# Kernel tuning notes

Measured on AMD Instinct MI355X. Metric: run time of the kernel, lower is better.

Reference implementation:

```python
import math
import jax, jax.numpy as jnp
import numpy as np


def _expmap0(u):
    # geoopt Lorentz (k=1) expmap0 followed by projection back onto the hyperboloid.
    # Minkowski norm of the tangent input (geoopt clamps at 1e-8 before sqrt).
    u0 = u[..., :1]
    us = u[..., 1:]
    mink = -u0 * u0 + jnp.sum(us * us, axis=-1, keepdims=True)
    nomin = jnp.sqrt(jnp.maximum(mink, 1e-8))
    r = jnp.sinh(nomin) * u / nomin
    space = r[..., 1:]
    time = jnp.sqrt(1.0 + jnp.sum(space * space, axis=-1, keepdims=True))  # project()
    return jnp.concatenate([time, space], axis=-1)


def setup_inputs() -> dict:
    key = jax.random.key(0)
    B, T, E, H = 2, 1024, 1024, 16
    ks = jax.random.split(key, 8)
    s = 0.02
    return {
        "x": jax.random.normal(ks[0], (B, T, E), jnp.float32),
        "Wqkv": jax.random.normal(ks[1], (3 * E, E), jnp.float32) * s,
        "bqkv": jnp.zeros((3 * E,), jnp.float32),
        "Wout": jax.random.normal(ks[2], (E, E), jnp.float32) * s,
        "bout": jnp.zeros((E,), jnp.float32),
        "Wimp": jax.random.normal(ks[3], (1, E), jnp.float32) * s,
        "bimp": jnp.zeros((1,), jnp.float32),
        "Walpha": jax.random.normal(ks[4], (H, E), jnp.float32) * s,
        "balpha": jnp.zeros((H,), jnp.float32),
        "spike_threshold": jnp.asarray(0.5, jnp.float32),
        "log_k": jnp.full((H,), 0.54, jnp.float32),
        "qk_scale": jnp.asarray(0.1, jnp.float32),
    }


def reference(x, Wqkv, bqkv, Wout, bout, Wimp, bimp, Walpha, balpha,
              spike_threshold, log_k, qk_scale):
    B, T, C = x.shape
    H = log_k.shape[0]
    D = C // H

    importance = jax.nn.sigmoid(x @ Wimp.T + bimp)          # (B,T,1)
    # torch.tril on the (T,1) trailing dims keeps every element -> no-op mask.
    spikes = (importance > spike_threshold).astype(x.dtype)
    spike_mask = spikes.reshape(B, 1, T, 1)

    alpha = jax.nn.sigmoid(x @ Walpha.T + balpha)           # (B,T,H)
    alpha = jnp.transpose(alpha, (0, 2, 1))[..., None]      # (B,H,T,1)

    qkv = (x @ Wqkv.T + bqkv).reshape(B, T, 3, H, D)
    q = jnp.transpose(qkv[:, :, 0], (0, 2, 1, 3))           # (B,H,T,D)
    k = jnp.transpose(qkv[:, :, 1], (0, 2, 1, 3))
    v = jnp.transpose(qkv[:, :, 2], (0, 2, 1, 3))

    scores_euclid = jnp.einsum('bhtd,bhsd->bhts', q, k) / math.sqrt(D)

    safe_scale = jax.nn.sigmoid(qk_scale) * 1.5
    qn = q / jnp.maximum(jnp.linalg.norm(q, axis=-1, keepdims=True), 1e-12) * safe_scale
    kn = k / jnp.maximum(jnp.linalg.norm(k, axis=-1, keepdims=True), 1e-12) * safe_scale
    q_hyp = _expmap0(qn)
    k_hyp = _expmap0(kn)

    inner = (-jnp.einsum('bhti,bhsi->bhts', q_hyp[..., :1], k_hyp[..., :1])
             + jnp.einsum('bhtd,bhsd->bhts', q_hyp[..., 1:], k_hyp[..., 1:]))
    curv_k = (jax.nn.softplus(log_k) + 1e-6).reshape(1, H, 1, 1)
    mdot = jnp.maximum(-inner, 1.0 + 1e-6)
    dist = jnp.arccosh(mdot)
    scores_hyper = -(dist * dist) / curv_k

    scores = (1.0 - alpha) * scores_euclid + alpha * scores_hyper
    causal = jnp.tril(jnp.ones((T, T), bool))
    scores = jnp.where(causal[None, None], scores, -jnp.inf)

    attn = jax.nn.softmax(scores, axis=-1) * spike_mask     # dropout disabled (eval)
    y = jnp.einsum('bhts,bhsd->bhtd', attn, v)
    y = jnp.transpose(y, (0, 2, 1, 3)).reshape(B, T, C)
    return y @ Wout.T + bout
```

## Files before the change

kernel.cpp:

```cpp
#include <hip/hip_runtime.h>
#include <math.h>

#define B_ 2
#define T_ 1024
#define E_ 1024
#define H_ 16
#define D_ 64
#define M_ (B_*T_)
#define SPLANE 32768

typedef __bf16 bf16x8 __attribute__((ext_vector_type(8)));
typedef __bf16 bf16x4 __attribute__((ext_vector_type(4)));
typedef __bf16 bf16x2 __attribute__((ext_vector_type(2)));
typedef float f32x4 __attribute__((ext_vector_type(4)));

__device__ __forceinline__ void* ldsp(__bf16* base, int row, int byte) {
  return (char*)base + row * 128 + (byte ^ ((row & 7) << 4));
}

__device__ __forceinline__ void gload_lds16(const void* g, void* l) {
  __builtin_amdgcn_global_load_lds((const __attribute__((address_space(1))) void*)g,
                                   (__attribute__((address_space(3))) void*)l, 16, 0, 0);
}

#define XV4 524288
#define WQV4 786432
#define WOV4 262144
#define TOTV4 (XV4 + WQV4 + WOV4)
__global__ __launch_bounds__(256) void conv_kernel(
    const float* __restrict__ x, const float* __restrict__ Wqkv,
    const float* __restrict__ Wout,
    __bf16* __restrict__ xb, __bf16* __restrict__ Wqkvb, __bf16* __restrict__ Woutb) {
  for (size_t i = (size_t)blockIdx.x * blockDim.x + threadIdx.x; i < TOTV4;
       i += (size_t)gridDim.x * blockDim.x) {
    const float4* src; __bf16* dst; size_t off;
    if (i < XV4)            { src = (const float4*)x;    dst = xb;    off = i; }
    else if (i < XV4+WQV4)  { src = (const float4*)Wqkv; dst = Wqkvb; off = i - XV4; }
    else                    { src = (const float4*)Wout; dst = Woutb; off = i - XV4 - WQV4; }
    float4 val = src[off];
    bf16x4 o = {(__bf16)val.x, (__bf16)val.y, (__bf16)val.z, (__bf16)val.w};
    *(bf16x4*)(dst + off * 4) = o;
  }
}

__global__ __launch_bounds__(256) void imp_alpha_kernel(
    const float* __restrict__ x,
    const float* __restrict__ Wimp, const float* __restrict__ bimp,
    const float* __restrict__ Walpha, const float* __restrict__ balpha,
    const float* __restrict__ thr_p,
    float* __restrict__ spike, float* __restrict__ alpha) {
  int m = blockIdx.x;
  int tid = threadIdx.x;
  const float4* xr = (const float4*)(x + (size_t)m * E_);
  float4 xv = xr[tid];
  float part[17];
  {
    float4 wv = ((const float4*)Wimp)[tid];
    part[16] = xv.x * wv.x + xv.y * wv.y + xv.z * wv.z + xv.w * wv.w;
  }
#pragma unroll
  for (int h = 0; h < 16; ++h) {
    float4 wv = ((const float4*)(Walpha + (size_t)h * E_))[tid];
    part[h] = xv.x * wv.x + xv.y * wv.y + xv.z * wv.z + xv.w * wv.w;
  }
  __shared__ float red[17][4];
  int lane = tid & 63, wv_ = tid >> 6;
#pragma unroll
  for (int i = 0; i < 17; ++i) {
    float v = part[i];
    for (int off = 32; off > 0; off >>= 1) v += __shfl_down(v, off, 64);
    if (lane == 0) red[i][wv_] = v;
  }
  __syncthreads();
  if (tid < 17) {
    float v = red[tid][0] + red[tid][1] + red[tid][2] + red[tid][3];
    if (tid == 16) {
      float z = v + bimp[0];
      float sig = 1.f / (1.f + expf(-z));
      spike[m] = (sig > thr_p[0]) ? 1.f : 0.f;
    } else {
      float z = v + balpha[tid];
      float a = 1.f / (1.f + expf(-z));
      int b = m >> 10, t = m & (T_ - 1);
      alpha[((size_t)(b * H_ + tid)) * T_ + t] = a;
    }
  }
}

__global__ __launch_bounds__(256) void qkv_gemm_kernel(
    const __bf16* __restrict__ A, const __bf16* __restrict__ Bm,
    const float* __restrict__ bias,
    __bf16* __restrict__ q, __bf16* __restrict__ k, __bf16* __restrict__ v) {
  __shared__ __bf16 As[128 * 32];
  __shared__ __bf16 Bs[128 * 32];
  const int K = E_;
  int tid = threadIdx.x;
  int w = tid >> 6, lane = tid & 63, lr = lane & 15, g = lane >> 4;
  int m0 = blockIdx.y * 128, n0 = blockIdx.x * 128;
  int wr = (w >> 1) * 64, wc = (w & 1) * 64;

  int task0 = tid, task1 = tid + 256;
  int r0s = task0 >> 2, c0s = task0 & 3;
  int r1s = task1 >> 2, c1s = task1 & 3;
  const __bf16* gA0 = A + (size_t)(m0 + r0s) * K + c0s * 8;
  const __bf16* gA1 = A + (size_t)(m0 + r1s) * K + c1s * 8;
  const __bf16* gB0 = Bm + (size_t)(n0 + r0s) * K + c0s * 8;
  const __bf16* gB1 = Bm + (size_t)(n0 + r1s) * K + c1s * 8;
  __bf16* lA0 = As + task0 * 8;
  __bf16* lA1 = As + task1 * 8;
  __bf16* lB0 = Bs + task0 * 8;
  __bf16* lB1 = Bs + task1 * 8;

  f32x4 acc[4][4];
#pragma unroll
  for (int i = 0; i < 4; ++i)
#pragma unroll
    for (int j = 0; j < 4; ++j) acc[i][j] = (f32x4){0.f, 0.f, 0.f, 0.f};

  for (int k0 = 0; k0 < K; k0 += 32) {
    gload_lds16(gA0, lA0); gload_lds16(gA1, lA1);
    gload_lds16(gB0, lB0); gload_lds16(gB1, lB1);
    gA0 += 32; gA1 += 32; gB0 += 32; gB1 += 32;
    __syncthreads();
    bf16x8 af[4], bf[4];
#pragma unroll
    for (int i = 0; i < 4; ++i) af[i] = *(bf16x8*)&As[(wr + i * 16 + lr) * 32 + g * 8];
#pragma unroll
    for (int j = 0; j < 4; ++j) bf[j] = *(bf16x8*)&Bs[(wc + j * 16 + lr) * 32 + g * 8];
#pragma unroll
    for (int i = 0; i < 4; ++i)
#pragma unroll
      for (int j = 0; j < 4; ++j)
        acc[i][j] = __builtin_amdgcn_mfma_f32_16x16x32_bf16(af[i], bf[j], acc[i][j], 0, 0, 0);
    __syncthreads();
  }

#pragma unroll
  for (int i = 0; i < 4; ++i) {
#pragma unroll
    for (int r = 0; r < 4; ++r) {
      int m = m0 + wr + i * 16 + g * 4 + r;
      int b = m >> 10, t = m & (T_ - 1);
#pragma unroll
      for (int j = 0; j < 4; ++j) {
        int n = n0 + wc + j * 16 + lr;
        float val = acc[i][j][r] + bias[n];
        int comp = n >> 10, h = (n >> 6) & 15, d = n & 63;
        __bf16* dst = (comp == 0) ? q : ((comp == 1) ? k : v);
        dst[(((size_t)(b * H_ + h)) * T_ + t) * 64 + d] = (__bf16)val;
      }
    }
  }
}

__global__ __launch_bounds__(256) void scal_kernel(
    const __bf16* __restrict__ q, const __bf16* __restrict__ k,
    const float* __restrict__ qk_scale_p,
    float* __restrict__ scalq, float* __restrict__ scalk) {
  int wid = blockIdx.x * 4 + (threadIdx.x >> 6);
  int lane = threadIdx.x & 63;
  int is_k = wid >> 15;
  int row = wid & 32767;
  const __bf16* src = (is_k ? k : q) + (size_t)row * 64;
  float u = (float)src[lane];
  float nsq = u * u;
#pragma unroll
  for (int off = 32; off > 0; off >>= 1) nsq += __shfl_xor(nsq, off, 64);
  float norm = fmaxf(sqrtf(nsq), 1e-12f);
  float ss = 1.5f / (1.f + expf(-qk_scale_p[0]));
  float row0 = __shfl(u, 0, 64);
  float un0 = row0 / norm * ss;
  float mink = ss * ss - 2.f * un0 * un0;
  float nu = sqrtf(fmaxf(mink, 1e-8f));
  float sc = sinhf(nu) / nu;
  float Bv = sc * ss / norm;
  float Av = sqrtf(1.f + sc * sc * (ss * ss - un0 * un0));
  float Cv = Bv * row0;
  if (lane == 0) {
    float* dst = is_k ? scalk : scalq;
    dst[row] = Av;
    dst[SPLANE + row] = Bv;
    dst[2 * SPLANE + row] = Cv;
  }
}

__global__ __launch_bounds__(256) void attn_kernel(
    const __bf16* __restrict__ q, const __bf16* __restrict__ k, const __bf16* __restrict__ v,
    const float* __restrict__ scalq, const float* __restrict__ scalk,
    const float* __restrict__ alpha, const float* __restrict__ log_k,
    __bf16* __restrict__ pacc, float* __restrict__ pml) {
  __shared__ __bf16 k_s[64 * 64];
  __shared__ __bf16 vt_s[64 * 64];
  __shared__ __bf16 p_s[64 * 64];

  int bid = blockIdx.x;
  int bh = ((bid & 7) << 2) | ((bid >> 3) & 3);
  int rest = bid >> 5;
  int qt = rest & 15;
  int half = rest >> 4;
  int h = bh & 15;
  int t0 = qt * 64;
  int n_st = qt + 1;
  int nh = (n_st + 1) >> 1;
  int s_beg = half ? nh : 0;
  int s_end = half ? n_st : nh;

  int tid = threadIdx.x;
  int w = tid >> 6, lane = tid & 63;
  int lr = lane & 15, g = lane >> 4;
  int trow = w * 16;
  const size_t base = (size_t)bh * T_ * 64;

  const __bf16* qrow = q + base + (size_t)(t0 + trow + lr) * 64;
  bf16x8 aq0 = *(const bf16x8*)(qrow + g * 8);
  bf16x8 aq1 = *(const bf16x8*)(qrow + 32 + g * 8);

  float curv = log1pf(expf(log_k[h])) + 1e-6f;
  float hc = 0.69314718056f / curv;
  const float ec = 0.18033688f;
  int tg[4]; float al[4], Aq[4], Bq[4], Cq[4];
#pragma unroll
  for (int r = 0; r < 4; ++r) {
    tg[r] = t0 + trow + g * 4 + r;
    int rowi = (bh << 10) + tg[r];
    al[r] = alpha[(size_t)bh * T_ + tg[r]];
    Aq[r] = scalq[rowi];
    Bq[r] = scalq[SPLANE + rowi];
    Cq[r] = scalq[2 * SPLANE + rowi];
  }

  float m_r[4] = {-1e30f, -1e30f, -1e30f, -1e30f};
  float l_r[4] = {0.f, 0.f, 0.f, 0.f};
  f32x4 acc[4];
#pragma unroll
  for (int n = 0; n < 4; ++n) acc[n] = (f32x4){0.f, 0.f, 0.f, 0.f};

  int task0 = tid, task1 = tid + 256;
  int row0s = task0 >> 3, cj0 = task0 & 7;
  int row1s = task1 >> 3, cj1 = task1 & 7;
  int s2 = tid & 31, dc = tid >> 5;

  for (int st = s_beg; st < s_end; ++st) {
    int s0 = st * 64;
    bool diag = (st == n_st - 1);
    __syncthreads();
    {
      bf16x8 a0 = *(const bf16x8*)(k + base + (size_t)(s0 + row0s) * 64 + cj0 * 8);
      bf16x8 a1 = *(const bf16x8*)(k + base + (size_t)(s0 + row1s) * 64 + cj1 * 8);
      *(bf16x8*)ldsp(k_s, row0s, cj0 * 16) = a0;
      *(bf16x8*)ldsp(k_s, row1s, cj1 * 16) = a1;
      bf16x8 v0 = *(const bf16x8*)(v + base + (size_t)(s0 + 2 * s2) * 64 + dc * 8);
      bf16x8 v1 = *(const bf16x8*)(v + base + (size_t)(s0 + 2 * s2 + 1) * 64 + dc * 8);
#pragma unroll
      for (int i = 0; i < 8; ++i) {
        bf16x2 pr = {v0[i], v1[i]};
        *(bf16x2*)ldsp(vt_s, dc * 8 + i, s2 * 4) = pr;
      }
    }
    __syncthreads();

    float pv[4][4];
    float pmax[4] = {-1e30f, -1e30f, -1e30f, -1e30f};
#pragma unroll
    for (int j = 0; j < 4; ++j) {
      if (diag && (s0 + j * 16 > t0 + trow + 15)) {
#pragma unroll
        for (int r = 0; r < 4; ++r) pv[j][r] = -1e30f;
        continue;
      }
      bf16x8 bk0 = *(bf16x8*)ldsp(k_s, j * 16 + lr, g * 16);
      bf16x8 bk1 = *(bf16x8*)ldsp(k_s, j * 16 + lr, 64 + g * 16);
      f32x4 z = {0.f, 0.f, 0.f, 0.f};
      z = __builtin_amdgcn_mfma_f32_16x16x32_bf16(aq0, bk0, z, 0, 0, 0);
      f32x4 se = __builtin_amdgcn_mfma_f32_16x16x32_bf16(aq1, bk1, z, 0, 0, 0);
      int sg = s0 + j * 16 + lr;
      int coli = (bh << 10) + sg;
      float ak = scalk[coli];
      float bk = scalk[SPLANE + coli];
      float ck = scalk[2 * SPLANE + coli];
#pragma unroll
      for (int r = 0; r < 4; ++r) {
        float dot = se[r];
        float sc_e = dot * ec;
        float md = fmaf(-Bq[r] * bk, dot, fmaf(Aq[r], ak, Cq[r] * ck));
        md = fmaxf(md, 1.0f + 1e-6f);
        float l2 = __log2f(md + sqrtf(fmaf(md, md, -1.f)));
        float t = fmaf(l2 * l2, hc, sc_e);
        float s = fmaf(-al[r], t, sc_e);
        if (diag && sg > tg[r]) s = -1e30f;
        pv[j][r] = s;
        pmax[r] = fmaxf(pmax[r], s);
      }
    }
#pragma unroll
    for (int r = 0; r < 4; ++r) {
      float mx = pmax[r];
      mx = fmaxf(mx, __shfl_xor(mx, 1, 64));
      mx = fmaxf(mx, __shfl_xor(mx, 2, 64));
      mx = fmaxf(mx, __shfl_xor(mx, 4, 64));
      mx = fmaxf(mx, __shfl_xor(mx, 8, 64));
      float mn = fmaxf(m_r[r], mx);
      float fac = exp2f(m_r[r] - mn);
      m_r[r] = mn;
      float ls = 0.f;
#pragma unroll
      for (int j = 0; j < 4; ++j) { pv[j][r] = exp2f(pv[j][r] - mn); ls += pv[j][r]; }
      ls += __shfl_xor(ls, 1, 64);
      ls += __shfl_xor(ls, 2, 64);
      ls += __shfl_xor(ls, 4, 64);
      ls += __shfl_xor(ls, 8, 64);
      l_r[r] = l_r[r] * fac + ls;
#pragma unroll
      for (int n = 0; n < 4; ++n) acc[n][r] *= fac;
    }
#pragma unroll
    for (int j = 0; j < 4; ++j)
#pragma unroll
      for (int r = 0; r < 4; ++r)
        *(__bf16*)ldsp(p_s, trow + g * 4 + r, (j * 16 + lr) * 2) = (__bf16)pv[j][r];
    bf16x8 ap0 = *(bf16x8*)ldsp(p_s, trow + lr, g * 16);
    bf16x8 ap1 = *(bf16x8*)ldsp(p_s, trow + lr, 64 + g * 16);
#pragma unroll
    for (int n = 0; n < 4; ++n) {
      bf16x8 bv0 = *(bf16x8*)ldsp(vt_s, n * 16 + lr, g * 16);
      bf16x8 bv1 = *(bf16x8*)ldsp(vt_s, n * 16 + lr, 64 + g * 16);
      acc[n] = __builtin_amdgcn_mfma_f32_16x16x32_bf16(ap0, bv0, acc[n], 0, 0, 0);
      acc[n] = __builtin_amdgcn_mfma_f32_16x16x32_bf16(ap1, bv1, acc[n], 0, 0, 0);
    }
  }

  int qt16 = (qt << 2) | w;
  int pidx = ((bh << 6) + qt16) * 2 + half;
  __bf16* pa = pacc + (size_t)pidx * 1024;
#pragma unroll
  for (int n = 0; n < 4; ++n)
#pragma unroll
    for (int r = 0; r < 4; ++r)
      pa[(g * 4 + r) * 64 + n * 16 + lr] = (__bf16)acc[n][r];
  if (lr == 0) {
#pragma unroll
    for (int r = 0; r < 4; ++r) {
      pml[(size_t)pidx * 32 + g * 4 + r] = m_r[r];
      pml[(size_t)pidx * 32 + 16 + g * 4 + r] = l_r[r];
    }
  }
}

__global__ __launch_bounds__(256) void merge_kernel(
    const __bf16* __restrict__ pacc, const float* __restrict__ pml,
    const float* __restrict__ spike, __bf16* __restrict__ yw) {
  int tid = threadIdx.x;
  int w = tid >> 6, lane = tid & 63;
  int wid = blockIdx.x * 4 + w;
  int bh = wid & 31;
  int qt = wid >> 5;
  int b = bh >> 4, h = bh & 15;
  size_t i1 = ((size_t)(bh << 6) + qt) * 2;
  size_t i2 = i1 + 1;
  const __bf16* a1 = pacc + i1 * 1024;
  const __bf16* a2 = pacc + i2 * 1024;
#pragma unroll 4
  for (int row = 0; row < 16; ++row) {
    float m1 = pml[i1 * 32 + row], l1 = pml[i1 * 32 + 16 + row];
    float m2 = pml[i2 * 32 + row], l2 = pml[i2 * 32 + 16 + row];
    float mm = fmaxf(m1, m2);
    float f1 = exp2f(m1 - mm), f2 = exp2f(m2 - mm);
    float l = l1 * f1 + l2 * f2;
    int t = qt * 16 + row;
    float iv = spike[(size_t)b * T_ + t] / l;
    float val = ((float)a1[row * 64 + lane] * f1 +
                 (float)a2[row * 64 + lane] * f2) * iv;
    yw[(size_t)(b * T_ + t) * E_ + h * 64 + lane] = (__bf16)val;
  }
}

__global__ __launch_bounds__(256) void out_gemm_kernel(
    const __bf16* __restrict__ A, const __bf16* __restrict__ Bm,
    const float* __restrict__ bias, float* __restrict__ outp) {
  __shared__ __bf16 As[128 * 32];
  __shared__ __bf16 Bs[128 * 32];
  const int K = E_;
  int tid = threadIdx.x;
  int w = tid >> 6, lane = tid & 63, lr = lane & 15, g = lane >> 4;
  int m0 = blockIdx.y * 128, n0 = blockIdx.x * 128;
  int wr = (w >> 1) * 64, wc = (w & 1) * 64;

  int task0 = tid, task1 = tid + 256;
  int r0s = task0 >> 2, c0s = task0 & 3;
  int r1s = task1 >> 2, c1s = task1 & 3;
  const __bf16* gA0 = A + (size_t)(m0 + r0s) * K + c0s * 8;
  const __bf16* gA1 = A + (size_t)(m0 + r1s) * K + c1s * 8;
  const __bf16* gB0 = Bm + (size_t)(n0 + r0s) * K + c0s * 8;
  const __bf16* gB1 = Bm + (size_t)(n0 + r1s) * K + c1s * 8;
  __bf16* lA0 = As + task0 * 8;
  __bf16* lA1 = As + task1 * 8;
  __bf16* lB0 = Bs + task0 * 8;
  __bf16* lB1 = Bs + task1 * 8;

  f32x4 acc[4][4];
#pragma unroll
  for (int i = 0; i < 4; ++i)
#pragma unroll
    for (int j = 0; j < 4; ++j) acc[i][j] = (f32x4){0.f, 0.f, 0.f, 0.f};

  for (int k0 = 0; k0 < K; k0 += 32) {
    gload_lds16(gA0, lA0); gload_lds16(gA1, lA1);
    gload_lds16(gB0, lB0); gload_lds16(gB1, lB1);
    gA0 += 32; gA1 += 32; gB0 += 32; gB1 += 32;
    __syncthreads();
    bf16x8 af[4], bf[4];
#pragma unroll
    for (int i = 0; i < 4; ++i) af[i] = *(bf16x8*)&As[(wr + i * 16 + lr) * 32 + g * 8];
#pragma unroll
    for (int j = 0; j < 4; ++j) bf[j] = *(bf16x8*)&Bs[(wc + j * 16 + lr) * 32 + g * 8];
#pragma unroll
    for (int i = 0; i < 4; ++i)
#pragma unroll
      for (int j = 0; j < 4; ++j)
        acc[i][j] = __builtin_amdgcn_mfma_f32_16x16x32_bf16(af[i], bf[j], acc[i][j], 0, 0, 0);
    __syncthreads();
  }

#pragma unroll
  for (int i = 0; i < 4; ++i) {
#pragma unroll
    for (int r = 0; r < 4; ++r) {
      int m = m0 + wr + i * 16 + g * 4 + r;
#pragma unroll
      for (int j = 0; j < 4; ++j) {
        int n = n0 + wc + j * 16 + lr;
        outp[(size_t)m * E_ + n] = acc[i][j][r] + bias[n];
      }
    }
  }
}

extern "C" void kernel_launch(void* const* d_in, const int* in_sizes, int n_in,
                              void* d_out, int out_size, void* d_ws, size_t ws_size,
                              hipStream_t stream) {
  const float* x      = (const float*)d_in[0];
  const float* Wqkv   = (const float*)d_in[1];
  const float* bqkv   = (const float*)d_in[2];
  const float* Wout   = (const float*)d_in[3];
  const float* bout   = (const float*)d_in[4];
  const float* Wimp   = (const float*)d_in[5];
  const float* bimp   = (const float*)d_in[6];
  const float* Walpha = (const float*)d_in[7];
  const float* balpha = (const float*)d_in[8];
  const float* thr    = (const float*)d_in[9];
  const float* log_k  = (const float*)d_in[10];
  const float* qk_sc  = (const float*)d_in[11];
  float* out = (float*)d_out;

  char* ws = (char*)d_ws;
  size_t off = 0;
  auto alloc = [&](size_t bytes) -> void* {
    void* p = (void*)(ws + off);
    off += (bytes + 255) & ~(size_t)255;
    return p;
  };
  const size_t qkv_elems = (size_t)B_ * H_ * T_ * D_;
  __bf16* xb    = (__bf16*)alloc((size_t)M_ * E_ * 2);
  __bf16* Wqkvb = (__bf16*)alloc((size_t)3 * E_ * E_ * 2);
  __bf16* Woutb = (__bf16*)alloc((size_t)E_ * E_ * 2);
  __bf16* q   = (__bf16*)alloc(qkv_elems * 2);
  __bf16* k   = (__bf16*)alloc(qkv_elems * 2);
  __bf16* v   = (__bf16*)alloc(qkv_elems * 2);
  __bf16* yw  = (__bf16*)alloc((size_t)M_ * E_ * 2);
  float* alphaw = (float*)alloc((size_t)B_ * H_ * T_ * sizeof(float));
  float* spikew = (float*)alloc((size_t)M_ * sizeof(float));
  float* pml    = (float*)alloc((size_t)4096 * 32 * sizeof(float));
  float* scalq  = (float*)alloc((size_t)3 * SPLANE * sizeof(float));
  float* scalk  = (float*)alloc((size_t)3 * SPLANE * sizeof(float));
  __bf16* pacc = (__bf16*)ws;

  conv_kernel<<<1024, 256, 0, stream>>>(x, Wqkv, Wout, xb, Wqkvb, Woutb);
  imp_alpha_kernel<<<M_, 256, 0, stream>>>(x, Wimp, bimp, Walpha, balpha, thr,
                                           spikew, alphaw);
  qkv_gemm_kernel<<<dim3(24, 16), 256, 0, stream>>>(xb, Wqkvb, bqkv, q, k, v);
  scal_kernel<<<(2 * B_ * H_ * T_) / 4, 256, 0, stream>>>(q, k, qk_sc, scalq, scalk);
  attn_kernel<<<1024, 256, 0, stream>>>(q, k, v, scalq, scalk, alphaw, log_k,
                                        pacc, pml);
  merge_kernel<<<512, 256, 0, stream>>>(pacc, pml, spikew, yw);
  out_gemm_kernel<<<dim3(8, 16), 256, 0, stream>>>(yw, Woutb, bout, out);
}
```

Baseline: 165.0 us.

## Split attention KV range into fixed 4-tile chunks with up-to-4-way merge

Replaces the two-way half split of each query tile's causal KV range with chunks of at most four 64-wide KV tiles, giving 40 work items per head and 1280 blocks, so per-block work is more balanced. The merge kernel now combines up to four partial (m, l, acc) results per row instead of two. The per-column scalk loads are hoisted ahead of the LDS staging, and the attention kernel gets a minimum-occupancy launch bound. The risks are more partial-result traffic and merge work, more register pressure from the occupancy bound, and the pml buffer growing to match.

```diff
diff --git a/kernel.cpp b/kernel.cpp
--- a/kernel.cpp
+++ b/kernel.cpp
@@ -21,6 +21,11 @@
 __device__ __forceinline__ void gload_lds16(const void* g, void* l) {
   __builtin_amdgcn_global_load_lds((const __attribute__((address_space(1))) void*)g,
                                    (__attribute__((address_space(3))) void*)l, 16, 0, 0);
+}
+
+__device__ __forceinline__ int qoff(int qt) {
+  int a = qt >> 2, r = qt & 3;
+  return qt + 2 * a * (a - 1) + a * r;
 }
 
 #define XV4 524288
@@ -184,7 +189,7 @@
   }
 }
 
-__global__ __launch_bounds__(256) void attn_kernel(
+__global__ __launch_bounds__(256, 5) void attn_kernel(
     const __bf16* __restrict__ q, const __bf16* __restrict__ k, const __bf16* __restrict__ v,
     const float* __restrict__ scalq, const float* __restrict__ scalk,
     const float* __restrict__ alpha, const float* __restrict__ log_k,
@@ -195,15 +200,18 @@
 
   int bid = blockIdx.x;
   int bh = ((bid & 7) << 2) | ((bid >> 3) & 3);
-  int rest = bid >> 5;
-  int qt = rest & 15;
-  int half = rest >> 4;
+  int l = bid >> 5;
+  int qt = 0, ii = 0;
+#pragma unroll
+  for (int u = 0; u < 16; ++u) {
+    int offu = qoff(u);
+    int nqu = (u >> 2) + 1;
+    if (l >= offu && l < offu + nqu) { qt = u; ii = l - offu; }
+  }
   int h = bh & 15;
   int t0 = qt * 64;
-  int n_st = qt + 1;
-  int nh = (n_st + 1) >> 1;
-  int s_beg = half ? nh : 0;
-  int s_end = half ? n_st : nh;
+  int s_beg = ii * 4;
+  int s_end = min(ii * 4 + 4, qt + 1);
 
   int tid = threadIdx.x;
   int w = tid >> 6, lane = tid & 63;
@@ -242,8 +250,16 @@
 
   for (int st = s_beg; st < s_end; ++st) {
     int s0 = st * 64;
-    bool diag = (st == n_st - 1);
+    bool diag = (st == qt);
     __syncthreads();
+    float akv[4], bkv[4], ckv[4];
+#pragma unroll
+    for (int j = 0; j < 4; ++j) {
+      int coli = (bh << 10) + s0 + j * 16 + lr;
+      akv[j] = scalk[coli];
+      bkv[j] = scalk[SPLANE + coli];
+      ckv[j] = scalk[2 * SPLANE + coli];
+    }
     {
       bf16x8 a0 = *(const bf16x8*)(k + base + (size_t)(s0 + row0s) * 64 + cj0 * 8);
       bf16x8 a1 = *(const bf16x8*)(k + base + (size_t)(s0 + row1s) * 64 + cj1 * 8);
@@ -274,15 +290,11 @@
       z = __builtin_amdgcn_mfma_f32_16x16x32_bf16(aq0, bk0, z, 0, 0, 0);
       f32x4 se = __builtin_amdgcn_mfma_f32_16x16x32_bf16(aq1, bk1, z, 0, 0, 0);
       int sg = s0 + j * 16 + lr;
-      int coli = (bh << 10) + sg;
-      float ak = scalk[coli];
-      float bk = scalk[SPLANE + coli];
-      float ck = scalk[2 * SPLANE + coli];
 #pragma unroll
       for (int r = 0; r < 4; ++r) {
         float dot = se[r];
         float sc_e = dot * ec;
-        float md = fmaf(-Bq[r] * bk, dot, fmaf(Aq[r], ak, Cq[r] * ck));
+        float md = fmaf(-Bq[r] * bkv[j], dot, fmaf(Aq[r], akv[j], Cq[r] * ckv[j]));
         md = fmaxf(md, 1.0f + 1e-6f);
         float l2 = __log2f(md + sqrtf(fmaf(md, md, -1.f)));
         float t = fmaf(l2 * l2, hc, sc_e);
@@ -329,8 +341,7 @@
     }
   }
 
-  int qt16 = (qt << 2) | w;
-  int pidx = ((bh << 6) + qt16) * 2 + half;
+  int pidx = ((bh * 40 + qoff(qt) + ii) << 2) | w;
   __bf16* pa = pacc + (size_t)pidx * 1024;
 #pragma unroll
   for (int n = 0; n < 4; ++n)
@@ -353,24 +364,36 @@
   int w = tid >> 6, lane = tid & 63;
   int wid = blockIdx.x * 4 + w;
   int bh = wid & 31;
-  int qt = wid >> 5;
+  int qt16 = wid >> 5;
   int b = bh >> 4, h = bh & 15;
-  size_t i1 = ((size_t)(bh << 6) + qt) * 2;
-  size_t i2 = i1 + 1;
-  const __bf16* a1 = pacc + i1 * 1024;
-  const __bf16* a2 = pacc + i2 * 1024;
-#pragma unroll 4
+  int qt = qt16 >> 2, wsub = qt16 & 3;
+  int nq = (qt >> 2) + 1;
+  int offq = qoff(qt);
+  int pp[4];
+#pragma unroll
+  for (int i = 0; i < 4; ++i)
+    pp[i] = ((bh * 40 + offq + min(i, nq - 1)) << 2) | wsub;
+
   for (int row = 0; row < 16; ++row) {
-    float m1 = pml[i1 * 32 + row], l1 = pml[i1 * 32 + 16 + row];
-    float m2 = pml[i2 * 32 + row], l2 = pml[i2 * 32 + 16 + row];
-    float mm = fmaxf(m1, m2);
-    float f1 = exp2f(m1 - mm), f2 = exp2f(m2 - mm);
-    float l = l1 * f1 + l2 * f2;
-    int t = qt * 16 + row;
-    float iv = spike[(size_t)b * T_ + t] / l;
-    float val = ((float)a1[row * 64 + lane] * f1 +
-                 (float)a2[row * 64 + lane] * f2) * iv;
-    yw[(size_t)(b * T_ + t) * E_ + h * 64 + lane] = (__bf16)val;
+    float mm = -1e30f;
+    float mv[4];
+#pragma unroll
+    for (int i = 0; i < 4; ++i) {
+      mv[i] = (i < nq) ? pml[(size_t)pp[i] * 32 + row] : -1e30f;
+      mm = fmaxf(mm, mv[i]);
+    }
+    float lsum = 0.f, val = 0.f;
+#pragma unroll
+    for (int i = 0; i < 4; ++i) {
+      if (i < nq) {
+        float f = exp2f(mv[i] - mm);
+        lsum += pml[(size_t)pp[i] * 32 + 16 + row] * f;
+        val += (float)pacc[(size_t)pp[i] * 1024 + row * 64 + lane] * f;
+      }
+    }
+    int t = qt16 * 16 + row;
+    float iv = spike[(size_t)b * T_ + t] / lsum;
+    yw[(size_t)(b * T_ + t) * E_ + h * 64 + lane] = (__bf16)(val * iv);
   }
 }
 
@@ -469,7 +492,7 @@
   __bf16* yw  = (__bf16*)alloc((size_t)M_ * E_ * 2);
   float* alphaw = (float*)alloc((size_t)B_ * H_ * T_ * sizeof(float));
   float* spikew = (float*)alloc((size_t)M_ * sizeof(float));
-  float* pml    = (float*)alloc((size_t)4096 * 32 * sizeof(float));
+  float* pml    = (float*)alloc((size_t)5120 * 32 * sizeof(float));
   float* scalq  = (float*)alloc((size_t)3 * SPLANE * sizeof(float));
   float* scalk  = (float*)alloc((size_t)3 * SPLANE * sizeof(float));
   __bf16* pacc = (__bf16*)ws;
@@ -479,7 +502,7 @@
                                            spikew, alphaw);
   qkv_gemm_kernel<<<dim3(24, 16), 256, 0, stream>>>(xb, Wqkvb, bqkv, q, k, v);
   scal_kernel<<<(2 * B_ * H_ * T_) / 4, 256, 0, stream>>>(q, k, qk_sc, scalq, scalk);
-  attn_kernel<<<1024, 256, 0, stream>>>(q, k, v, scalq, scalk, alphaw, log_k,
+  attn_kernel<<<1280, 256, 0, stream>>>(q, k, v, scalq, scalk, alphaw, log_k,
                                         pacc, pml);
   merge_kernel<<<512, 256, 0, stream>>>(pacc, pml, spikew, yw);
   out_gemm_kernel<<<dim3(8, 16), 256, 0, stream>>>(yw, Woutb, bout, out);
```

Measured after the change: 221.5 us. +34.2%, slower.
